# Performance work log

Measured on AMD Instinct MI355X. Metric: run time of the kernel, lower is better.

The kernel has to match this reference:

```python
import jax, jax.numpy as jnp
import numpy as np


def setup_inputs() -> dict:
    key = jax.random.key(0)
    N = 100000
    x = jax.random.normal(key, (N,), dtype=jnp.float32)
    return {"x": x, "f_true": 90, "fs": 100000, "delta": 3, "f_min": 40, "f_max": 240}


def reference(x, f_true, fs, delta, f_min, f_max):
    # PSD(f) = (sum_i x[i] cos(2*pi*f*i/fs))^2 + (sum_i x[i] sin(2*pi*f*i/fs))^2
    # evaluated at integer frequencies f in [f_min, f_max]; loss = -10*log10(sum_wanted / sum_unwanted)
    N = x.shape[0]
    freqs = jnp.arange(f_min, f_max + 1)                      # [F] int bins
    t = jnp.arange(N, dtype=jnp.float32)                      # [N]
    ang = (2.0 * jnp.pi / fs) * freqs.astype(jnp.float32)[:, None] * t[None, :]  # [F, N]
    real = jnp.cos(ang) @ x                                   # [F]
    imag = jnp.sin(ang) @ x                                   # [F]
    psd = real * real + imag * imag                           # [F]
    wanted = (freqs >= f_true - delta) & (freqs <= f_true + delta)
    term1 = jnp.sum(jnp.where(wanted, psd, 0.0))
    term2 = jnp.sum(jnp.where(wanted, 0.0, psd))
    return -10.0 * jnp.log10(term1 / term2)
```

## Files before the change

### kernel.cpp

```cpp
#include <hip/hip_runtime.h>
#include <math.h>

#define BLK   256
#define MAXF  512
#define SPLIT 8
#define ILP   4

__global__ void __launch_bounds__(BLK) dft_proj_kernel(
    const float* __restrict__ x, int N,
    const int* __restrict__ p_fs,
    const int* __restrict__ p_fmin,
    const int* __restrict__ p_fmax,
    float* __restrict__ ws)
{
    const unsigned fs   = (unsigned)*p_fs;
    const int      fmin = *p_fmin;
    const int      fmax = *p_fmax;
    const int      F    = fmax - fmin + 1;
    const float  inv_fs = 1.0f / (float)fs;

    const int Nc = (N + SPLIT - 1) / SPLIT;
    const int W  = F * SPLIT;

    float* re = ws;
    float* im = ws + MAXF * SPLIT;

    __shared__ float red[8];

    for (int w = blockIdx.x; w < W; w += gridDim.x) {
        const int j     = w >> 3;
        const int chunk = w & (SPLIT - 1);
        if (j >= MAXF) break;

        const unsigned f   = (unsigned)(fmin + j);
        const int      tid = threadIdx.x;
        const int      i0  = chunk * Nc + tid;
        const int      iend = min(N, (chunk + 1) * Nc);

        const unsigned kb = (unsigned)(((unsigned long long)f * (unsigned)(chunk * Nc)) % fs);
        const unsigned sb = (f * (unsigned)BLK) % fs;
        unsigned pt = (f * (unsigned)tid) % fs;
        unsigned k0 = kb + pt; if (k0 >= fs) k0 -= fs;

        unsigned k[ILP];
        k[0] = k0;
        #pragma unroll
        for (int u = 1; u < ILP; ++u) { k[u] = k[u-1] + sb; if (k[u] >= fs) k[u] -= fs; }
        unsigned sL = sb;
        #pragma unroll
        for (int r = 0; r < 2; ++r) { sL += sL; if (sL >= fs) sL -= fs; }

        float c[ILP], s[ILP], ar[ILP], ai[ILP];
        #pragma unroll
        for (int u = 0; u < ILP; ++u) {
            float rev = (float)k[u] * inv_fs;
            s[u] = __builtin_amdgcn_sinf(rev);
            c[u] = __builtin_amdgcn_cosf(rev);
            ar[u] = 0.0f; ai[u] = 0.0f;
        }
        float revL = (float)sL * inv_fs;
        const float S = __builtin_amdgcn_sinf(revL);
        const float C = __builtin_amdgcn_cosf(revL);

        int i = i0;
        for (; i + (ILP - 1) * BLK < iend; i += ILP * BLK) {
            #pragma unroll
            for (int u = 0; u < ILP; ++u) {
                float xv = x[i + u * BLK];
                ar[u] = fmaf(xv, c[u], ar[u]);
                ai[u] = fmaf(xv, s[u], ai[u]);
                float cn = fmaf(c[u], C, -(s[u] * S));
                float sn = fmaf(s[u], C,  (c[u] * S));
                c[u] = cn; s[u] = sn;
            }
        }
        #pragma unroll
        for (int u = 0; u < ILP; ++u) {
            int idx = i + u * BLK;
            if (idx < iend) {
                float xv = x[idx];
                ar[u] = fmaf(xv, c[u], ar[u]);
                ai[u] = fmaf(xv, s[u], ai[u]);
            }
        }

        float arS = (ar[0] + ar[1]) + (ar[2] + ar[3]);
        float aiS = (ai[0] + ai[1]) + (ai[2] + ai[3]);

        #pragma unroll
        for (int o = 32; o > 0; o >>= 1) {
            arS += __shfl_down(arS, o, 64);
            aiS += __shfl_down(aiS, o, 64);
        }
        const int lane = tid & 63;
        const int wid  = tid >> 6;
        if (lane == 0) { red[wid * 2] = arS; red[wid * 2 + 1] = aiS; }
        __syncthreads();
        if (tid == 0) {
            re[w] = (red[0] + red[2]) + (red[4] + red[6]);
            im[w] = (red[1] + red[3]) + (red[5] + red[7]);
        }
        __syncthreads();
    }
}

__global__ void __launch_bounds__(BLK) loss_kernel(
    const float* __restrict__ ws,
    const int* __restrict__ p_ftrue,
    const int* __restrict__ p_delta,
    const int* __restrict__ p_fmin,
    const int* __restrict__ p_fmax,
    float* __restrict__ out)
{
    const int ftrue = *p_ftrue;
    const int delta = *p_delta;
    const int fmin  = *p_fmin;
    const int fmax  = *p_fmax;
    const int F     = fmax - fmin + 1;

    float t1 = 0.0f, t2 = 0.0f;
    for (int j = threadIdx.x; j < F && j < MAXF; j += BLK) {
        float r = 0.0f, m = 0.0f;
        #pragma unroll
        for (int u = 0; u < SPLIT; ++u) {
            r += ws[j * SPLIT + u];
            m += ws[MAXF * SPLIT + j * SPLIT + u];
        }
        float psd = r * r + m * m;
        int   fq  = fmin + j;
        bool wanted = (fq >= ftrue - delta) && (fq <= ftrue + delta);
        if (wanted) t1 += psd; else t2 += psd;
    }

    __shared__ float red[8];
    #pragma unroll
    for (int o = 32; o > 0; o >>= 1) {
        t1 += __shfl_down(t1, o, 64);
        t2 += __shfl_down(t2, o, 64);
    }
    const int lane = threadIdx.x & 63;
    const int wid  = threadIdx.x >> 6;
    if (lane == 0) { red[wid * 2] = t1; red[wid * 2 + 1] = t2; }
    __syncthreads();
    if (threadIdx.x == 0) {
        float a = (red[0] + red[2]) + (red[4] + red[6]);
        float b = (red[1] + red[3]) + (red[5] + red[7]);
        out[0] = -10.0f * log10f(a / b);
    }
}

extern "C" void kernel_launch(void* const* d_in, const int* in_sizes, int n_in,
                              void* d_out, int out_size, void* d_ws, size_t ws_size,
                              hipStream_t stream) {
    const float* x       = (const float*)d_in[0];
    const int*   p_ftrue = (const int*)d_in[1];
    const int*   p_fs    = (const int*)d_in[2];
    const int*   p_delta = (const int*)d_in[3];
    const int*   p_fmin  = (const int*)d_in[4];
    const int*   p_fmax  = (const int*)d_in[5];
    float*       out     = (float*)d_out;
    float*       ws      = (float*)d_ws;
    const int N = in_sizes[0];

    dft_proj_kernel<<<2048, BLK, 0, stream>>>(x, N, p_fs, p_fmin, p_fmax, ws);
    loss_kernel<<<1, BLK, 0, stream>>>(ws, p_ftrue, p_delta, p_fmin, p_fmax, out);
}
```

Baseline: 14.51 us.

## Vectorize DFT inner loop with float4 loads and per-lane phase accumulators

Each thread now reads four consecutive samples with a float4 load and keeps four separate complex accumulators, one per sub-phase. The accumulators are rotated by e^{i k f} only at the end, so one twiddle recurrence serves four samples and trig and rotation work per sample drops. SPLIT goes from 8 to 4, the grid from 2048 to 1024 blocks, and a float-reciprocal modulo replaces one integer modulo. The trade-off is fewer blocks for parallelism and longer recurrence chains per thread, which may cost some rotation accuracy.

```diff
diff --git a/kernel.cpp b/kernel.cpp
--- a/kernel.cpp
+++ b/kernel.cpp
@@ -3,8 +3,17 @@
 
 #define BLK   256
 #define MAXF  512
-#define SPLIT 8
-#define ILP   4
+#define SPLIT 4
+
+__device__ __forceinline__ unsigned umod_fast(unsigned a, unsigned fs, float inv_fs) {
+    unsigned q = (unsigned)((float)a * inv_fs);
+    int r = (int)a - (int)(q * fs);
+    if (r < 0) r += (int)fs;
+    if (r < 0) r += (int)fs;
+    if (r >= (int)fs) r -= (int)fs;
+    if (r >= (int)fs) r -= (int)fs;
+    return (unsigned)r;
+}
 
 __global__ void __launch_bounds__(BLK) dft_proj_kernel(
     const float* __restrict__ x, int N,
@@ -19,8 +28,9 @@
     const int      F    = fmax - fmin + 1;
     const float  inv_fs = 1.0f / (float)fs;
 
-    const int Nc = (N + SPLIT - 1) / SPLIT;
-    const int W  = F * SPLIT;
+    int Nc = (N + SPLIT - 1) / SPLIT;
+    Nc = (Nc + 3) & ~3;
+    const int W = F * SPLIT;
 
     float* re = ws;
     float* im = ws + MAXF * SPLIT;
@@ -28,64 +38,88 @@
     __shared__ float red[8];
 
     for (int w = blockIdx.x; w < W; w += gridDim.x) {
-        const int j     = w >> 3;
+        const int j     = w >> 2;
         const int chunk = w & (SPLIT - 1);
         if (j >= MAXF) break;
 
         const unsigned f   = (unsigned)(fmin + j);
         const int      tid = threadIdx.x;
-        const int      i0  = chunk * Nc + tid;
-        const int      iend = min(N, (chunk + 1) * Nc);
-
-        const unsigned kb = (unsigned)(((unsigned long long)f * (unsigned)(chunk * Nc)) % fs);
-        const unsigned sb = (f * (unsigned)BLK) % fs;
-        unsigned pt = (f * (unsigned)tid) % fs;
+        const int      cs   = chunk * Nc;
+        const int      iend = min(N, cs + Nc);
+
+        const unsigned kb = (unsigned)(((unsigned long long)f * (unsigned)cs) % fs);
+        unsigned pt = umod_fast(f * (unsigned)(4 * tid), fs, inv_fs);
         unsigned k0 = kb + pt; if (k0 >= fs) k0 -= fs;
-
-        unsigned k[ILP];
-        k[0] = k0;
-        #pragma unroll
-        for (int u = 1; u < ILP; ++u) { k[u] = k[u-1] + sb; if (k[u] >= fs) k[u] -= fs; }
-        unsigned sL = sb;
-        #pragma unroll
-        for (int r = 0; r < 2; ++r) { sL += sL; if (sL >= fs) sL -= fs; }
-
-        float c[ILP], s[ILP], ar[ILP], ai[ILP];
-        #pragma unroll
-        for (int u = 0; u < ILP; ++u) {
-            float rev = (float)k[u] * inv_fs;
-            s[u] = __builtin_amdgcn_sinf(rev);
-            c[u] = __builtin_amdgcn_cosf(rev);
-            ar[u] = 0.0f; ai[u] = 0.0f;
-        }
-        float revL = (float)sL * inv_fs;
-        const float S = __builtin_amdgcn_sinf(revL);
-        const float C = __builtin_amdgcn_cosf(revL);
-
-        int i = i0;
-        for (; i + (ILP - 1) * BLK < iend; i += ILP * BLK) {
-            #pragma unroll
-            for (int u = 0; u < ILP; ++u) {
-                float xv = x[i + u * BLK];
-                ar[u] = fmaf(xv, c[u], ar[u]);
-                ai[u] = fmaf(xv, s[u], ai[u]);
-                float cn = fmaf(c[u], C, -(s[u] * S));
-                float sn = fmaf(s[u], C,  (c[u] * S));
-                c[u] = cn; s[u] = sn;
-            }
-        }
-        #pragma unroll
-        for (int u = 0; u < ILP; ++u) {
-            int idx = i + u * BLK;
+        const unsigned k4 = (unsigned)(((unsigned long long)f * (unsigned)(4 * BLK)) % fs);
+        const unsigned kf = (f >= fs) ? (f % fs) : f;
+
+        float cA = __builtin_amdgcn_cosf((float)k0 * inv_fs);
+        float sA = __builtin_amdgcn_sinf((float)k0 * inv_fs);
+        const float C4 = __builtin_amdgcn_cosf((float)k4 * inv_fs);
+        const float S4 = __builtin_amdgcn_sinf((float)k4 * inv_fs);
+        float cB = fmaf(cA, C4, -(sA * S4));
+        float sB = fmaf(sA, C4,  (cA * S4));
+        const float C8 = fmaf(C4, C4, -(S4 * S4));
+        const float S8 = 2.0f * C4 * S4;
+
+        float a0r = 0.f, a0i = 0.f, a1r = 0.f, a1i = 0.f;
+        float a2r = 0.f, a2i = 0.f, a3r = 0.f, a3i = 0.f;
+
+        int b = cs + 4 * tid;
+        for (; b + 4 * BLK + 4 <= iend; b += 8 * BLK) {
+            float4 xa = *reinterpret_cast<const float4*>(x + b);
+            float4 xb = *reinterpret_cast<const float4*>(x + b + 4 * BLK);
+            a0r = fmaf(xa.x, cA, a0r); a0i = fmaf(xa.x, sA, a0i);
+            a1r = fmaf(xa.y, cA, a1r); a1i = fmaf(xa.y, sA, a1i);
+            a2r = fmaf(xa.z, cA, a2r); a2i = fmaf(xa.z, sA, a2i);
+            a3r = fmaf(xa.w, cA, a3r); a3i = fmaf(xa.w, sA, a3i);
+            a0r = fmaf(xb.x, cB, a0r); a0i = fmaf(xb.x, sB, a0i);
+            a1r = fmaf(xb.y, cB, a1r); a1i = fmaf(xb.y, sB, a1i);
+            a2r = fmaf(xb.z, cB, a2r); a2i = fmaf(xb.z, sB, a2i);
+            a3r = fmaf(xb.w, cB, a3r); a3i = fmaf(xb.w, sB, a3i);
+            float cn = fmaf(cA, C8, -(sA * S8));
+            float sn = fmaf(sA, C8,  (cA * S8));
+            cA = cn; sA = sn;
+            cn = fmaf(cB, C8, -(sB * S8));
+            sn = fmaf(sB, C8,  (cB * S8));
+            cB = cn; sB = sn;
+        }
+        #pragma unroll
+        for (int p = 0; p < 4; ++p) {
+            int idx = b + p;
             if (idx < iend) {
                 float xv = x[idx];
-                ar[u] = fmaf(xv, c[u], ar[u]);
-                ai[u] = fmaf(xv, s[u], ai[u]);
+                if (p == 0) { a0r = fmaf(xv, cA, a0r); a0i = fmaf(xv, sA, a0i); }
+                if (p == 1) { a1r = fmaf(xv, cA, a1r); a1i = fmaf(xv, sA, a1i); }
+                if (p == 2) { a2r = fmaf(xv, cA, a2r); a2i = fmaf(xv, sA, a2i); }
+                if (p == 3) { a3r = fmaf(xv, cA, a3r); a3i = fmaf(xv, sA, a3i); }
             }
         }
-
-        float arS = (ar[0] + ar[1]) + (ar[2] + ar[3]);
-        float aiS = (ai[0] + ai[1]) + (ai[2] + ai[3]);
+        #pragma unroll
+        for (int p = 0; p < 4; ++p) {
+            int idx = b + 4 * BLK + p;
+            if (idx < iend) {
+                float xv = x[idx];
+                if (p == 0) { a0r = fmaf(xv, cB, a0r); a0i = fmaf(xv, sB, a0i); }
+                if (p == 1) { a1r = fmaf(xv, cB, a1r); a1i = fmaf(xv, sB, a1i); }
+                if (p == 2) { a2r = fmaf(xv, cB, a2r); a2i = fmaf(xv, sB, a2i); }
+                if (p == 3) { a3r = fmaf(xv, cB, a3r); a3i = fmaf(xv, sB, a3i); }
+            }
+        }
+
+        const float c1 = __builtin_amdgcn_cosf((float)kf * inv_fs);
+        const float s1 = __builtin_amdgcn_sinf((float)kf * inv_fs);
+        const float c2 = fmaf(c1, c1, -(s1 * s1));
+        const float s2 = 2.0f * c1 * s1;
+        const float c3 = fmaf(c2, c1, -(s2 * s1));
+        const float s3 = fmaf(s2, c1,  (c2 * s1));
+        float arS = a0r, aiS = a0i;
+        arS = fmaf(c1, a1r, arS); arS = fmaf(-s1, a1i, arS);
+        aiS = fmaf(c1, a1i, aiS); aiS = fmaf( s1, a1r, aiS);
+        arS = fmaf(c2, a2r, arS); arS = fmaf(-s2, a2i, arS);
+        aiS = fmaf(c2, a2i, aiS); aiS = fmaf( s2, a2r, aiS);
+        arS = fmaf(c3, a3r, arS); arS = fmaf(-s3, a3i, arS);
+        aiS = fmaf(c3, a3i, aiS); aiS = fmaf( s3, a3r, aiS);
 
         #pragma unroll
         for (int o = 32; o > 0; o >>= 1) {
@@ -162,6 +196,6 @@
     float*       ws      = (float*)d_ws;
     const int N = in_sizes[0];
 
-    dft_proj_kernel<<<2048, BLK, 0, stream>>>(x, N, p_fs, p_fmin, p_fmax, ws);
+    dft_proj_kernel<<<1024, BLK, 0, stream>>>(x, N, p_fs, p_fmin, p_fmax, ws);
     loss_kernel<<<1, BLK, 0, stream>>>(ws, p_ftrue, p_delta, p_fmin, p_fmax, out);
 }
```

New measurement: 12.58 us. -13.3%, faster.
